# Optimization experiments

Hardware: AMD Instinct MI355X
Metric: run time of the kernel (lower is better)

The kernel has to match this reference:

```python
import jax, jax.numpy as jnp
import numpy as np

D = 512
N_TISSUES = 200
N_MECH = 6
WINDOW = 32
LN_EPS = 1e-5


def _make_params(key):
    ks = jax.random.split(key, 16)
    p = {}
    def lin(k, fin, fout):
        return jax.random.normal(k, (fin, fout), jnp.float32) * 0.02, jnp.zeros((fout,), jnp.float32)
    for s in ('local', 'regional', 'macro'):
        p[f'ln_g_{s}'] = jnp.ones((D,), jnp.float32)
        p[f'ln_b_{s}'] = jnp.zeros((D,), jnp.float32)
    p['W_fuse'], p['b_fuse'] = lin(ks[0], 3 * D, D)
    p['W_i1'], p['b_i1'] = lin(ks[1], D, D // 2)
    p['W_i2'], p['b_i2'] = lin(ks[2], D // 2, 1)
    p['W_t1'], p['b_t1'] = lin(ks[3], D, D)
    p['W_t2'], p['b_t2'] = lin(ks[4], D, N_TISSUES)
    p['W_m1'], p['b_m1'] = lin(ks[5], D, D // 2)
    p['W_m2'], p['b_m2'] = lin(ks[6], D // 2, N_MECH)
    return p


def setup_inputs() -> dict:
    key = jax.random.key(0)
    ks = jax.random.split(key, 8)
    B, L = 16, 4096
    inp = {}
    names = ['ref_local', 'ref_regional', 'ref_macro', 'alt_local', 'alt_regional', 'alt_macro']
    for i, n in enumerate(names):
        inp[n] = jax.random.normal(ks[i], (B, L, D), jnp.float32)
    inp['variant_pos'] = jax.random.randint(ks[6], (B,), 0, L, jnp.int32)
    inp.update(_make_params(ks[7]))
    return inp


def _diff_pool(ref, alt, pos, gamma, beta):
    # Vectorized version of the per-batch boundary-clamped window gather:
    # window [pos-w, pos+w] intersected with [0, L), diff = alt-ref, mean-pool.
    B, L, Dm = ref.shape
    offs = jnp.arange(-WINDOW, WINDOW + 1)          # (2w+1,)
    idx = pos[:, None] + offs[None, :]               # (B, 2w+1)
    valid = (idx >= 0) & (idx < L)                   # boundary clamp mask
    idxc = jnp.clip(idx, 0, L - 1)
    r = jnp.take_along_axis(ref, idxc[:, :, None], axis=1)   # (B, 2w+1, D)
    a = jnp.take_along_axis(alt, idxc[:, :, None], axis=1)
    diff = (a - r) * valid[:, :, None].astype(ref.dtype)
    pooled = diff.sum(axis=1) / valid.sum(axis=1)[:, None].astype(ref.dtype)  # (B, D)
    mu = pooled.mean(axis=-1, keepdims=True)
    var = ((pooled - mu) ** 2).mean(axis=-1, keepdims=True)
    return (pooled - mu) / jnp.sqrt(var + LN_EPS) * gamma + beta


def _gelu(x):
    return jax.nn.gelu(x, approximate=False)


def reference(ref_local, ref_regional, ref_macro, alt_local, alt_regional, alt_macro,
              variant_pos,
              ln_g_local, ln_b_local, ln_g_regional, ln_b_regional, ln_g_macro, ln_b_macro,
              W_fuse, b_fuse, W_i1, b_i1, W_i2, b_i2,
              W_t1, b_t1, W_t2, b_t2, W_m1, b_m1, W_m2, b_m2):
    d_local = _diff_pool(ref_local, alt_local, variant_pos, ln_g_local, ln_b_local)
    d_reg = _diff_pool(ref_regional, alt_regional, variant_pos, ln_g_regional, ln_b_regional)
    d_mac = _diff_pool(ref_macro, alt_macro, variant_pos, ln_g_macro, ln_b_macro)
    cat = jnp.concatenate([d_local, d_reg, d_mac], axis=-1)   # (B, 3D)
    fused = _gelu(cat @ W_fuse + b_fuse)                       # (B, D); dropout = eval identity
    impact = jax.nn.sigmoid(_gelu(fused @ W_i1 + b_i1) @ W_i2 + b_i2)[:, 0]  # (B,)
    tissue = _gelu(fused @ W_t1 + b_t1) @ W_t2 + b_t2          # (B, n_tissues)
    mech = _gelu(fused @ W_m1 + b_m1) @ W_m2 + b_m2            # (B, 6)
    return impact, tissue, mech, fused
```

## Files before the change

### kernel.cpp

```cpp
#include <hip/hip_runtime.h>
#include <math.h>

#define D 512
#define LSEQ 4096
#define NB 16
#define WINDOW 32
#define NCHUNK 5
#define CHUNK 13
#define N_TISSUES 200
#define N_MECH 6
#define LN_EPS 1e-5f

#define WS_PARTIAL 0
#define WS_CAT     122880
#define WS_FUSED   147456
#define WS_H1      155648
#define WS_T2      172032
#define ZERO_SPAN  27776

__device__ __forceinline__ float gelu_exact(float x) {
    return 0.5f * x * (1.0f + erff(x * 0.70710678118654752f));
}
__device__ __forceinline__ void atom_add(float* p, float v) {
    unsafeAtomicAdd(p, v);
}

__global__ __launch_bounds__(256) void pool_partial_kernel(
    const float* __restrict__ ref0, const float* __restrict__ ref1, const float* __restrict__ ref2,
    const float* __restrict__ alt0, const float* __restrict__ alt1, const float* __restrict__ alt2,
    const int* __restrict__ pos, float* __restrict__ partial)
{
    const int blk = blockIdx.x;
    const int b = blk / (3 * NCHUNK);
    const int s = (blk / NCHUNK) % 3;
    const int c = blk % NCHUNK;
    const float* __restrict__ ref = (s == 0) ? ref0 : ((s == 1) ? ref1 : ref2);
    const float* __restrict__ alt = (s == 0) ? alt0 : ((s == 1) ? alt1 : alt2);
    const int p = pos[b];
    const int tid = threadIdx.x;

    float acc0 = 0.0f, acc1 = 0.0f;
    const int base_off = -WINDOW + c * CHUNK;
    #pragma unroll
    for (int i = 0; i < CHUNK; ++i) {
        const int idx = p + base_off + i;
        if (idx >= 0 && idx < LSEQ) {
            const size_t row = ((size_t)b * LSEQ + (size_t)idx) * D;
            acc0 += alt[row + tid]       - ref[row + tid];
            acc1 += alt[row + tid + 256] - ref[row + tid + 256];
        }
    }
    float* __restrict__ outp = partial + ((size_t)(b * 3 + s) * NCHUNK + c) * D;
    outp[tid]       = acc0;
    outp[tid + 256] = acc1;
}

__global__ __launch_bounds__(512) void prep_kernel(
    const float* __restrict__ partial, const int* __restrict__ pos,
    const float* __restrict__ g0, const float* __restrict__ be0,
    const float* __restrict__ g1, const float* __restrict__ be1,
    const float* __restrict__ g2, const float* __restrict__ be2,
    float* __restrict__ cat, float* __restrict__ zero_base)
{
    __shared__ float red[16];
    const int blk = blockIdx.x;
    const int b = blk / 3;
    const int s = blk % 3;
    const int tid = threadIdx.x;
    const int lane = tid & 63;
    const int wave = tid >> 6;

    for (int i = blk * 512 + tid; i < ZERO_SPAN; i += 48 * 512)
        zero_base[i] = 0.0f;

    const int p = pos[b];
    const int lo = (p - WINDOW < 0) ? 0 : (p - WINDOW);
    const int hi = (p + WINDOW > LSEQ - 1) ? (LSEQ - 1) : (p + WINDOW);
    const float inv_cnt = 1.0f / (float)(hi - lo + 1);

    const float* __restrict__ part = partial + (size_t)(b * 3 + s) * NCHUNK * D;
    float v = part[tid] + part[D + tid] + part[2 * D + tid]
            + part[3 * D + tid] + part[4 * D + tid];
    v *= inv_cnt;

    float s1 = v, s2 = v * v;
    #pragma unroll
    for (int o = 32; o > 0; o >>= 1) {
        s1 += __shfl_down(s1, o, 64);
        s2 += __shfl_down(s2, o, 64);
    }
    if (lane == 0) { red[wave] = s1; red[8 + wave] = s2; }
    __syncthreads();
    float t1_ = 0.0f, t2_ = 0.0f;
    #pragma unroll
    for (int w = 0; w < 8; ++w) { t1_ += red[w]; t2_ += red[8 + w]; }
    const float mu = t1_ * (1.0f / (float)D);
    const float var = t2_ * (1.0f / (float)D) - mu * mu;
    const float rstd = rsqrtf(var + LN_EPS);

    const float* __restrict__ g  = (s == 0) ? g0  : ((s == 1) ? g1  : g2);
    const float* __restrict__ be = (s == 0) ? be0 : ((s == 1) ? be1 : be2);
    cat[(size_t)b * 1536 + s * D + tid] = (v - mu) * rstd * g[tid] + be[tid];
}

__global__ __launch_bounds__(256) void fused_mm_kernel(
    const float* __restrict__ cat, const float* __restrict__ Wf,
    float* __restrict__ fused_raw)
{
    __shared__ float xl[16 * 64];
    const int kc = blockIdx.x >> 1;
    const int cg = blockIdx.x & 1;
    const int tid = threadIdx.x;

    {
        const int e = tid * 4;
        const int b = e >> 6, kk = e & 63;
        *(float4*)&xl[e] = *(const float4*)&cat[(size_t)b * 1536 + kc * 64 + kk];
    }
    __syncthreads();

    const int col = cg * 256 + tid;
    float acc[16];
    #pragma unroll
    for (int b = 0; b < 16; ++b) acc[b] = 0.0f;

    const float* __restrict__ wp = Wf + (size_t)(kc * 64) * D + col;
    #pragma unroll 4
    for (int kk = 0; kk < 64; ++kk) {
        const float w = wp[(size_t)kk * D];
        #pragma unroll
        for (int b = 0; b < 16; ++b) acc[b] += xl[b * 64 + kk] * w;
    }
    #pragma unroll
    for (int b = 0; b < 16; ++b) atom_add(&fused_raw[b * D + col], acc[b]);
}

__global__ __launch_bounds__(256) void h1_mm_kernel(
    const float* __restrict__ fused_raw, const float* __restrict__ bf,
    const float* __restrict__ Wt1, const float* __restrict__ Wi1,
    const float* __restrict__ Wm1,
    float* __restrict__ h1_raw, float* __restrict__ out)
{
    __shared__ float xl[16 * 64];
    const int kc = blockIdx.x >> 2;
    const int cg = blockIdx.x & 3;
    const int tid = threadIdx.x;

    {
        const int e = tid * 4;
        const int b = e >> 6, kk = e & 63;
        const float4 r = *(const float4*)&fused_raw[(size_t)b * D + kc * 64 + kk];
        const float4 bb = *(const float4*)&bf[kc * 64 + kk];
        float4 gg;
        gg.x = gelu_exact(r.x + bb.x); gg.y = gelu_exact(r.y + bb.y);
        gg.z = gelu_exact(r.z + bb.z); gg.w = gelu_exact(r.w + bb.w);
        *(float4*)&xl[e] = gg;
        if (cg == 0) *(float4*)&out[3312 + (size_t)b * D + kc * 64 + kk] = gg;
    }
    __syncthreads();

    const int col = cg * 256 + tid;
    const float* __restrict__ wp;
    int ldw;
    if (cg < 2)      { wp = Wt1 + (size_t)(kc * 64) * D + col;          ldw = D;   }
    else if (cg == 2){ wp = Wi1 + (size_t)(kc * 64) * 256 + (col - 512); ldw = 256; }
    else             { wp = Wm1 + (size_t)(kc * 64) * 256 + (col - 768); ldw = 256; }

    float acc[16];
    #pragma unroll
    for (int b = 0; b < 16; ++b) acc[b] = 0.0f;
    #pragma unroll 4
    for (int kk = 0; kk < 64; ++kk) {
        const float w = wp[(size_t)kk * ldw];
        #pragma unroll
        for (int b = 0; b < 16; ++b) acc[b] += xl[b * 64 + kk] * w;
    }
    #pragma unroll
    for (int b = 0; b < 16; ++b) atom_add(&h1_raw[b * 1024 + col], acc[b]);
}

__global__ __launch_bounds__(256) void small_heads_kernel(
    const float* __restrict__ h1_raw,
    const float* __restrict__ bt1, const float* __restrict__ bi1,
    const float* __restrict__ bm1,
    const float* __restrict__ Wt2, const float* __restrict__ Wm2,
    const float* __restrict__ Wi2, const float* __restrict__ bm2,
    const float* __restrict__ bi2,
    float* __restrict__ t2_raw, float* __restrict__ out)
{
    __shared__ float s[8192];
    const int tid = threadIdx.x;

    if (blockIdx.x < 8) {
        const int kc = blockIdx.x;
        {
            const int e = tid * 4;
            const int b = e >> 6, kk = e & 63;
            const float4 r = *(const float4*)&h1_raw[(size_t)b * 1024 + kc * 64 + kk];
            const float4 bb = *(const float4*)&bt1[kc * 64 + kk];
            s[e]     = gelu_exact(r.x + bb.x);
            s[e + 1] = gelu_exact(r.y + bb.y);
            s[e + 2] = gelu_exact(r.z + bb.z);
            s[e + 3] = gelu_exact(r.w + bb.w);
        }
        __syncthreads();
        if (tid < N_TISSUES) {
            const float* __restrict__ wp = Wt2 + (size_t)(kc * 64) * N_TISSUES + tid;
            float acc[16];
            #pragma unroll
            for (int b = 0; b < 16; ++b) acc[b] = 0.0f;
            #pragma unroll 4
            for (int kk = 0; kk < 64; ++kk) {
                const float w = wp[(size_t)kk * N_TISSUES];
                #pragma unroll
                for (int b = 0; b < 16; ++b) acc[b] += s[b * 64 + kk] * w;
            }
            #pragma unroll
            for (int b = 0; b < 16; ++b) atom_add(&t2_raw[b * N_TISSUES + tid], acc[b]);
        }
    } else {
        for (int b = 0; b < 16; ++b) {
            s[b * 256 + tid]        = gelu_exact(bi1[tid] + h1_raw[(size_t)b * 1024 + 512 + tid]);
            s[4096 + b * 256 + tid] = gelu_exact(bm1[tid] + h1_raw[(size_t)b * 1024 + 768 + tid]);
        }
        __syncthreads();
        if (tid < 96) {
            const int b = tid / 6, m = tid % 6;
            float a0 = 0, a1 = 0, a2 = 0, a3 = 0;
            for (int j = 0; j < 256; j += 4) {
                a0 += s[4096 + b * 256 + j]     * Wm2[(j)     * N_MECH + m];
                a1 += s[4096 + b * 256 + j + 1] * Wm2[(j + 1) * N_MECH + m];
                a2 += s[4096 + b * 256 + j + 2] * Wm2[(j + 2) * N_MECH + m];
                a3 += s[4096 + b * 256 + j + 3] * Wm2[(j + 3) * N_MECH + m];
            }
            out[3216 + tid] = bm2[m] + ((a0 + a1) + (a2 + a3));
        } else if (tid < 112) {
            const int b = tid - 96;
            float a0 = 0, a1 = 0, a2 = 0, a3 = 0;
            for (int j = 0; j < 256; j += 4) {
                a0 += s[b * 256 + j]     * Wi2[j];
                a1 += s[b * 256 + j + 1] * Wi2[j + 1];
                a2 += s[b * 256 + j + 2] * Wi2[j + 2];
                a3 += s[b * 256 + j + 3] * Wi2[j + 3];
            }
            const float x = bi2[0] + ((a0 + a1) + (a2 + a3));
            out[b] = 1.0f / (1.0f + expf(-x));
        }
    }
}

__global__ __launch_bounds__(256) void t2_final_kernel(
    const float* __restrict__ t2_raw, const float* __restrict__ bt2,
    float* __restrict__ out)
{
    const int gid = blockIdx.x * 256 + threadIdx.x;
    if (gid < NB * N_TISSUES) {
        const int c = gid % N_TISSUES;
        out[16 + gid] = bt2[c] + t2_raw[gid];
    }
}

extern "C" void kernel_launch(void* const* d_in, const int* in_sizes, int n_in,
                              void* d_out, int out_size, void* d_ws, size_t ws_size,
                              hipStream_t stream) {
    const float* ref_local    = (const float*)d_in[0];
    const float* ref_regional = (const float*)d_in[1];
    const float* ref_macro    = (const float*)d_in[2];
    const float* alt_local    = (const float*)d_in[3];
    const float* alt_regional = (const float*)d_in[4];
    const float* alt_macro    = (const float*)d_in[5];
    const int*   pos          = (const int*)d_in[6];
    const float* g0  = (const float*)d_in[7];
    const float* be0 = (const float*)d_in[8];
    const float* g1  = (const float*)d_in[9];
    const float* be1 = (const float*)d_in[10];
    const float* g2  = (const float*)d_in[11];
    const float* be2 = (const float*)d_in[12];
    const float* Wf  = (const float*)d_in[13];
    const float* bf  = (const float*)d_in[14];
    const float* Wi1 = (const float*)d_in[15];
    const float* bi1 = (const float*)d_in[16];
    const float* Wi2 = (const float*)d_in[17];
    const float* bi2 = (const float*)d_in[18];
    const float* Wt1 = (const float*)d_in[19];
    const float* bt1 = (const float*)d_in[20];
    const float* Wt2 = (const float*)d_in[21];
    const float* bt2 = (const float*)d_in[22];
    const float* Wm1 = (const float*)d_in[23];
    const float* bm1 = (const float*)d_in[24];
    const float* Wm2 = (const float*)d_in[25];
    const float* bm2 = (const float*)d_in[26];

    float* ws        = (float*)d_ws;
    float* partial   = ws + WS_PARTIAL;
    float* cat       = ws + WS_CAT;
    float* fused_raw = ws + WS_FUSED;
    float* h1_raw    = ws + WS_H1;
    float* t2_raw    = ws + WS_T2;
    float* out       = (float*)d_out;

    pool_partial_kernel<<<NB * 3 * NCHUNK, 256, 0, stream>>>(
        ref_local, ref_regional, ref_macro,
        alt_local, alt_regional, alt_macro, pos, partial);

    prep_kernel<<<48, 512, 0, stream>>>(
        partial, pos, g0, be0, g1, be1, g2, be2, cat, fused_raw );

    fused_mm_kernel<<<48, 256, 0, stream>>>(cat, Wf, fused_raw);

    h1_mm_kernel<<<32, 256, 0, stream>>>(fused_raw, bf, Wt1, Wi1, Wm1, h1_raw, out);

    small_heads_kernel<<<9, 256, 0, stream>>>(
        h1_raw, bt1, bi1, bm1, Wt2, Wm2, Wi2, bm2, bi2, t2_raw, out);

    t2_final_kernel<<<13, 256, 0, stream>>>(t2_raw, bt2, out);
}
```

Baseline: 553.5 us.

## Split pooling into more chunks, move zeroing into pool kernel, fuse tissue head

The pooling kernel now uses 10 chunks of 7 rows, giving 480 blocks instead of 240, and loads float2 per thread. Eight extra blocks zero the atomic accumulators, so the zeroing no longer sits in the prep kernel. The tissue head is recomputed in a 512-thread kernel where each thread does a full K=512 dot product and writes the biased output directly. This drops the t2 atomics and the separate t2_final launch, at the cost of less parallelism across K in the heads stage.

```diff
diff --git a/kernel.cpp b/kernel.cpp
--- a/kernel.cpp
+++ b/kernel.cpp
@@ -5,18 +5,17 @@
 #define LSEQ 4096
 #define NB 16
 #define WINDOW 32
-#define NCHUNK 5
-#define CHUNK 13
+#define NCHUNK 10
+#define CHUNK 7
 #define N_TISSUES 200
 #define N_MECH 6
 #define LN_EPS 1e-5f
 
 #define WS_PARTIAL 0
-#define WS_CAT     122880
-#define WS_FUSED   147456
-#define WS_H1      155648
-#define WS_T2      172032
-#define ZERO_SPAN  27776
+#define WS_CAT     245760
+#define WS_FUSED   270336
+#define WS_H1      278528
+#define ZERO_SPAN  24576
 
 __device__ __forceinline__ float gelu_exact(float x) {
     return 0.5f * x * (1.0f + erff(x * 0.70710678118654752f));
@@ -25,34 +24,44 @@
     unsafeAtomicAdd(p, v);
 }
 
-__global__ __launch_bounds__(256) void pool_partial_kernel(
+__global__ __launch_bounds__(256) void pool_zero_kernel(
     const float* __restrict__ ref0, const float* __restrict__ ref1, const float* __restrict__ ref2,
     const float* __restrict__ alt0, const float* __restrict__ alt1, const float* __restrict__ alt2,
-    const int* __restrict__ pos, float* __restrict__ partial)
+    const int* __restrict__ pos, float* __restrict__ partial,
+    float* __restrict__ zero_base)
 {
     const int blk = blockIdx.x;
-    const int b = blk / (3 * NCHUNK);
-    const int s = (blk / NCHUNK) % 3;
-    const int c = blk % NCHUNK;
+    const int tid = threadIdx.x;
+
+    if (blk >= 480) {
+        for (int i = (blk - 480) * 256 + tid; i < ZERO_SPAN; i += 8 * 256)
+            zero_base[i] = 0.0f;
+        return;
+    }
+
+    const int b = blk / 30;
+    const int r = blk % 30;
+    const int s = r / NCHUNK;
+    const int c = r % NCHUNK;
     const float* __restrict__ ref = (s == 0) ? ref0 : ((s == 1) ? ref1 : ref2);
     const float* __restrict__ alt = (s == 0) ? alt0 : ((s == 1) ? alt1 : alt2);
     const int p = pos[b];
-    const int tid = threadIdx.x;
 
     float acc0 = 0.0f, acc1 = 0.0f;
-    const int base_off = -WINDOW + c * CHUNK;
     #pragma unroll
     for (int i = 0; i < CHUNK; ++i) {
-        const int idx = p + base_off + i;
-        if (idx >= 0 && idx < LSEQ) {
+        const int j = c * CHUNK + i;
+        const int idx = p + j - WINDOW;
+        if (j < 65 && idx >= 0 && idx < LSEQ) {
             const size_t row = ((size_t)b * LSEQ + (size_t)idx) * D;
-            acc0 += alt[row + tid]       - ref[row + tid];
-            acc1 += alt[row + tid + 256] - ref[row + tid + 256];
+            const float2 a2 = *(const float2*)&alt[row + 2 * tid];
+            const float2 r2 = *(const float2*)&ref[row + 2 * tid];
+            acc0 += a2.x - r2.x;
+            acc1 += a2.y - r2.y;
         }
     }
-    float* __restrict__ outp = partial + ((size_t)(b * 3 + s) * NCHUNK + c) * D;
-    outp[tid]       = acc0;
-    outp[tid + 256] = acc1;
+    float2 o; o.x = acc0; o.y = acc1;
+    *(float2*)&partial[((size_t)(b * 3 + s) * NCHUNK + c) * D + 2 * tid] = o;
 }
 
 __global__ __launch_bounds__(512) void prep_kernel(
@@ -60,7 +69,7 @@
     const float* __restrict__ g0, const float* __restrict__ be0,
     const float* __restrict__ g1, const float* __restrict__ be1,
     const float* __restrict__ g2, const float* __restrict__ be2,
-    float* __restrict__ cat, float* __restrict__ zero_base)
+    float* __restrict__ cat)
 {
     __shared__ float red[16];
     const int blk = blockIdx.x;
@@ -70,17 +79,15 @@
     const int lane = tid & 63;
     const int wave = tid >> 6;
 
-    for (int i = blk * 512 + tid; i < ZERO_SPAN; i += 48 * 512)
-        zero_base[i] = 0.0f;
-
     const int p = pos[b];
     const int lo = (p - WINDOW < 0) ? 0 : (p - WINDOW);
     const int hi = (p + WINDOW > LSEQ - 1) ? (LSEQ - 1) : (p + WINDOW);
     const float inv_cnt = 1.0f / (float)(hi - lo + 1);
 
     const float* __restrict__ part = partial + (size_t)(b * 3 + s) * NCHUNK * D;
-    float v = part[tid] + part[D + tid] + part[2 * D + tid]
-            + part[3 * D + tid] + part[4 * D + tid];
+    float v = 0.0f;
+    #pragma unroll
+    for (int c = 0; c < NCHUNK; ++c) v += part[c * D + tid];
     v *= inv_cnt;
 
     float s1 = v, s2 = v * v;
@@ -162,7 +169,7 @@
     const int col = cg * 256 + tid;
     const float* __restrict__ wp;
     int ldw;
-    if (cg < 2)      { wp = Wt1 + (size_t)(kc * 64) * D + col;          ldw = D;   }
+    if (cg < 2)      { wp = Wt1 + (size_t)(kc * 64) * D + col;           ldw = D;   }
     else if (cg == 2){ wp = Wi1 + (size_t)(kc * 64) * 256 + (col - 512); ldw = 256; }
     else             { wp = Wm1 + (size_t)(kc * 64) * 256 + (col - 768); ldw = 256; }
 
@@ -179,51 +186,56 @@
     for (int b = 0; b < 16; ++b) atom_add(&h1_raw[b * 1024 + col], acc[b]);
 }
 
-__global__ __launch_bounds__(256) void small_heads_kernel(
+__global__ __launch_bounds__(512) void heads_kernel(
     const float* __restrict__ h1_raw,
     const float* __restrict__ bt1, const float* __restrict__ bi1,
     const float* __restrict__ bm1,
-    const float* __restrict__ Wt2, const float* __restrict__ Wm2,
-    const float* __restrict__ Wi2, const float* __restrict__ bm2,
-    const float* __restrict__ bi2,
-    float* __restrict__ t2_raw, float* __restrict__ out)
-{
-    __shared__ float s[8192];
+    const float* __restrict__ Wt2, const float* __restrict__ bt2,
+    const float* __restrict__ Wm2, const float* __restrict__ bm2,
+    const float* __restrict__ Wi2, const float* __restrict__ bi2,
+    float* __restrict__ out)
+{
+    __shared__ float s[16 * 516];
     const int tid = threadIdx.x;
 
     if (blockIdx.x < 8) {
-        const int kc = blockIdx.x;
-        {
-            const int e = tid * 4;
-            const int b = e >> 6, kk = e & 63;
-            const float4 r = *(const float4*)&h1_raw[(size_t)b * 1024 + kc * 64 + kk];
-            const float4 bb = *(const float4*)&bt1[kc * 64 + kk];
-            s[e]     = gelu_exact(r.x + bb.x);
-            s[e + 1] = gelu_exact(r.y + bb.y);
-            s[e + 2] = gelu_exact(r.z + bb.z);
-            s[e + 3] = gelu_exact(r.w + bb.w);
+        const float btc = bt1[tid];
+        #pragma unroll
+        for (int b = 0; b < 16; ++b)
+            s[b * 516 + tid] = gelu_exact(btc + h1_raw[(size_t)b * 1024 + tid]);
+        __syncthreads();
+
+        if (tid < 400) {
+            const int col_l = tid % 25;
+            const int b     = tid / 25;
+            const int col   = blockIdx.x * 25 + col_l;
+            const float* __restrict__ wp = Wt2 + col;
+            const float* __restrict__ xp = s + b * 516;
+            float a0 = 0, a1 = 0, a2 = 0, a3 = 0;
+            #pragma unroll 4
+            for (int k = 0; k < D; k += 4) {
+                a0 += xp[k]     * wp[(size_t)k * N_TISSUES];
+                a1 += xp[k + 1] * wp[(size_t)(k + 1) * N_TISSUES];
+                a2 += xp[k + 2] * wp[(size_t)(k + 2) * N_TISSUES];
+                a3 += xp[k + 3] * wp[(size_t)(k + 3) * N_TISSUES];
+            }
+            out[16 + b * N_TISSUES + col] = bt2[col] + ((a0 + a1) + (a2 + a3));
+        }
+    } else {
+        if (tid < 256) {
+            const float bic = bi1[tid];
+            #pragma unroll
+            for (int b = 0; b < 16; ++b)
+                s[b * 256 + tid] = gelu_exact(bic + h1_raw[(size_t)b * 1024 + 512 + tid]);
+        } else {
+            const int j = tid - 256;
+            const float bmc = bm1[j];
+            #pragma unroll
+            for (int b = 0; b < 16; ++b)
+                s[4096 + b * 256 + j] = gelu_exact(bmc + h1_raw[(size_t)b * 1024 + 768 + j]);
         }
         __syncthreads();
-        if (tid < N_TISSUES) {
-            const float* __restrict__ wp = Wt2 + (size_t)(kc * 64) * N_TISSUES + tid;
-            float acc[16];
-            #pragma unroll
-            for (int b = 0; b < 16; ++b) acc[b] = 0.0f;
-            #pragma unroll 4
-            for (int kk = 0; kk < 64; ++kk) {
-                const float w = wp[(size_t)kk * N_TISSUES];
-                #pragma unroll
-                for (int b = 0; b < 16; ++b) acc[b] += s[b * 64 + kk] * w;
-            }
-            #pragma unroll
-            for (int b = 0; b < 16; ++b) atom_add(&t2_raw[b * N_TISSUES + tid], acc[b]);
-        }
-    } else {
-        for (int b = 0; b < 16; ++b) {
-            s[b * 256 + tid]        = gelu_exact(bi1[tid] + h1_raw[(size_t)b * 1024 + 512 + tid]);
-            s[4096 + b * 256 + tid] = gelu_exact(bm1[tid] + h1_raw[(size_t)b * 1024 + 768 + tid]);
-        }
-        __syncthreads();
+
         if (tid < 96) {
             const int b = tid / 6, m = tid % 6;
             float a0 = 0, a1 = 0, a2 = 0, a3 = 0;
@@ -246,17 +258,6 @@
             const float x = bi2[0] + ((a0 + a1) + (a2 + a3));
             out[b] = 1.0f / (1.0f + expf(-x));
         }
-    }
-}
-
-__global__ __launch_bounds__(256) void t2_final_kernel(
-    const float* __restrict__ t2_raw, const float* __restrict__ bt2,
-    float* __restrict__ out)
-{
-    const int gid = blockIdx.x * 256 + threadIdx.x;
-    if (gid < NB * N_TISSUES) {
-        const int c = gid % N_TISSUES;
-        out[16 + gid] = bt2[c] + t2_raw[gid];
     }
 }
 
@@ -296,22 +297,19 @@
     float* cat       = ws + WS_CAT;
     float* fused_raw = ws + WS_FUSED;
     float* h1_raw    = ws + WS_H1;
-    float* t2_raw    = ws + WS_T2;
     float* out       = (float*)d_out;
 
-    pool_partial_kernel<<<NB * 3 * NCHUNK, 256, 0, stream>>>(
+    pool_zero_kernel<<<488, 256, 0, stream>>>(
         ref_local, ref_regional, ref_macro,
-        alt_local, alt_regional, alt_macro, pos, partial);
+        alt_local, alt_regional, alt_macro, pos, partial, fused_raw );
 
     prep_kernel<<<48, 512, 0, stream>>>(
-        partial, pos, g0, be0, g1, be1, g2, be2, cat, fused_raw );
+        partial, pos, g0, be0, g1, be1, g2, be2, cat);
 
     fused_mm_kernel<<<48, 256, 0, stream>>>(cat, Wf, fused_raw);
 
     h1_mm_kernel<<<32, 256, 0, stream>>>(fused_raw, bf, Wt1, Wi1, Wm1, h1_raw, out);
 
-    small_heads_kernel<<<9, 256, 0, stream>>>(
-        h1_raw, bt1, bi1, bm1, Wt2, Wm2, Wi2, bm2, bi2, t2_raw, out);
-
-    t2_final_kernel<<<13, 256, 0, stream>>>(t2_raw, bt2, out);
-}
+    heads_kernel<<<9, 512, 0, stream>>>(
+        h1_raw, bt1, bi1, bm1, Wt2, bt2, Wm2, bm2, Wi2, bi2, out);
+}
```

New measurement: 552.4 us. About the same (-0.2%).
